# Kernel optimization log

Hardware: AMD Instinct MI355X
Metric: run time of the kernel (lower is better)

## Reference

```python
import jax, jax.numpy as jnp
import numpy as np

B, S, P, V, D = 8, 32, 8, 8000, 128
CONC = 5.0  # concentrator_factor
EPS = 1e-8  # torch cosine_similarity eps


def setup_inputs() -> dict:
    key = jax.random.key(0)
    ks = jax.random.split(key, 8)
    concepts = jax.random.randint(ks[0], (B, S, P), 0, V)
    concepts_length = jax.random.randint(ks[1], (B, S), 0, P + 1)
    seg_len = jax.random.randint(ks[2], (B,), 1, S + 1)
    embed_w = jax.random.normal(ks[3], (V, D), jnp.float32)
    embed_kb_w = jax.random.normal(ks[4], (V, D), jnp.float32)
    edge_matrix = jax.random.uniform(ks[5], (V, V), jnp.float32)
    affectiveness = jax.random.uniform(ks[6], (V,), jnp.float32)
    lam = jnp.full((V,), 0.5, jnp.float32)  # _lambda init to GAW
    return dict(concepts=concepts, concepts_length=concepts_length, seg_len=seg_len,
                embed_w=embed_w, embed_kb_w=embed_kb_w, edge_matrix=edge_matrix,
                affectiveness=affectiveness, lam=lam)


def reference(concepts, concepts_length, seg_len, embed_w, embed_kb_w,
              edge_matrix, affectiveness, lam):
    f32 = embed_w.dtype
    # init_params: normalize edge_matrix rows by their range
    rng = edge_matrix.max(axis=1) - edge_matrix.min(axis=1)  # [V]
    em = edge_matrix / (rng + (rng == 0).astype(f32))[:, None]

    ce = embed_w[concepts]  # [B,S,P,D]
    # ragged mean over P (empty -> zeros, matching empty_tensor)
    pmask = (jnp.arange(P)[None, None, :] < concepts_length[:, :, None]).astype(f32)  # [B,S,P]
    denom = jnp.maximum(concepts_length, 1).astype(f32)[:, :, None]  # [B,S,1]
    mean_j = (ce * pmask[..., None]).sum(axis=2) / denom  # [B,S,D]
    # mean over valid segments j < seg_len
    smask = (jnp.arange(S)[None, :] < seg_len[:, None]).astype(f32)  # [B,S]
    context = (mean_j * smask[..., None]).sum(axis=1) / seg_len.astype(f32)[:, None]  # [B,D]

    # abs cosine similarity vs KB embedding table
    cn = context / jnp.maximum(jnp.linalg.norm(context, axis=1, keepdims=True), EPS)
    kn = embed_kb_w / jnp.maximum(jnp.linalg.norm(embed_kb_w, axis=1, keepdims=True), EPS)
    cos = jnp.abs(cn @ kn.T)  # [B,V]

    eg = em[concepts]  # [B,S,P,V] irregular row gather
    rel = eg * cos[:, None, None, :]
    aff = (eg > 0).astype(f32) * affectiveness
    w = lam * rel + (1.0 - lam) * aff  # [B,S,P,V]
    attn = jax.nn.softmax(w * CONC, axis=3)
    ce2 = attn @ embed_kb_w  # [B,S,P,D]

    # ragged mean over P again, zero out segments j >= seg_len (padded output)
    out = (ce2 * pmask[..., None]).sum(axis=2) / denom  # [B,S,D]
    out = out * smask[..., None]
    return out
```

## Files before the change

kernel.cpp:

```cpp
#include <hip/hip_runtime.h>
#include <cmath>

#define NB 8
#define NS 32
#define NP 8
#define NV 8000
#define ND 128
#define CONC 5.0f
#define EPS 1e-8f

#define TROWS 16
#define USPLIT 25
#define URANGE 320
#define UCHUNK 64
#define NCHUNK (URANGE / UCHUNK)
#define ST 20
#define MAXSLOTS (NB * NS * NP)

#define WS_CNT    0
#define WS_METAO  16
#define WS_SCALE  2064
#define WS_CN     4112
#define WS_COS    5136
#define WS_MEANJ  69136
#define WS_P      101904

__global__ void k_mean(const int* __restrict__ concepts,
                       const int* __restrict__ concepts_length,
                       const float* __restrict__ embed_w,
                       float* __restrict__ mean_j,
                       float* __restrict__ out,
                       int* __restrict__ counter) {
    const int bs = blockIdx.x;
    const int d = threadIdx.x;
    out[bs * ND + d] = 0.0f;
    if (bs == 0 && d == 0) counter[0] = 0;
    const int len = concepts_length[bs];
    float sum = 0.0f;
    for (int p = 0; p < len; ++p) {
        const int c = concepts[bs * NP + p];
        sum += embed_w[(size_t)c * ND + d];
    }
    mean_j[(size_t)bs * ND + d] = sum / (float)(len > 0 ? len : 1);
}

__global__ void k_ctx2(const int* __restrict__ seg_len,
                       const float* __restrict__ mean_j,
                       float* __restrict__ cn) {
    const int b = blockIdx.x;
    const int d = threadIdx.x;
    const int sl = seg_len[b];
    float acc = 0.0f;
    for (int s = 0; s < sl; ++s) acc += mean_j[(size_t)(b * NS + s) * ND + d];
    acc /= (float)sl;
    float ss = acc * acc;
    #pragma unroll
    for (int m = 1; m < 64; m <<= 1) ss += __shfl_xor(ss, m);
    __shared__ float sred[2];
    if ((d & 63) == 0) sred[d >> 6] = ss;
    __syncthreads();
    const float tot = sred[0] + sred[1];
    cn[b * ND + d] = acc / fmaxf(sqrtf(tot), EPS);
}

__global__ __launch_bounds__(256) void k_cos(const float* __restrict__ kb,
                                             const float* __restrict__ cn,
                                             float* __restrict__ cos_bv) {
    __shared__ float s_cn[NB * ND];
    const int t = threadIdx.x;
    for (int i = t; i < NB * ND; i += 256) s_cn[i] = cn[i];
    __syncthreads();

    const int v = blockIdx.x * 8 + (t >> 5);
    const int l = t & 31;
    const float4 kv = *reinterpret_cast<const float4*>(kb + (size_t)v * ND + (l << 2));
    float ss = kv.x * kv.x + kv.y * kv.y + kv.z * kv.z + kv.w * kv.w;
    #pragma unroll
    for (int m = 1; m < 32; m <<= 1) ss += __shfl_xor(ss, m);
    const float inv = 1.0f / fmaxf(sqrtf(ss), EPS);
    #pragma unroll
    for (int b = 0; b < NB; ++b) {
        const float4 cv = *reinterpret_cast<const float4*>(&s_cn[b * ND + (l << 2)]);
        float dot = kv.x * cv.x + kv.y * cv.y + kv.z * cv.z + kv.w * cv.w;
        #pragma unroll
        for (int m = 1; m < 32; m <<= 1) dot += __shfl_xor(dot, m);
        if (l == 0) cos_bv[b * NV + v] = fabsf(dot * inv);
    }
}

__global__ __launch_bounds__(256) void k_A(
        const int* __restrict__ concepts,
        const int* __restrict__ concepts_length,
        const int* __restrict__ seg_len,
        const float* __restrict__ edge,
        const float* __restrict__ aff,
        const float* __restrict__ lam,
        const float* __restrict__ cos_bv,
        int* __restrict__ counter,
        int* __restrict__ meta_out,
        float* __restrict__ f_scale,
        float* __restrict__ pbuf) {
    const int idx = blockIdx.x;
    const int b = idx >> 8;
    const int s = (idx >> 3) & 31;
    const int p = idx & 7;
    if (s >= seg_len[b]) return;
    const int len = concepts_length[b * NS + s];
    if (p >= len) return;
    const int c = concepts[idx];

    const int t = threadIdx.x;
    const float* __restrict__ erow = edge + (size_t)c * NV;
    float4 ev[8];
    float lmax = -INFINITY, lmin = INFINITY;
    #pragma unroll
    for (int k = 0; k < 8; ++k) {
        const int f = t + (k << 8);
        if (f < 2000) {
            const float4 e = *reinterpret_cast<const float4*>(erow + (f << 2));
            ev[k] = e;
            lmax = fmaxf(lmax, fmaxf(fmaxf(e.x, e.y), fmaxf(e.z, e.w)));
            lmin = fminf(lmin, fminf(fminf(e.x, e.y), fminf(e.z, e.w)));
        }
    }
    #pragma unroll
    for (int m = 1; m < 64; m <<= 1) {
        lmax = fmaxf(lmax, __shfl_xor(lmax, m));
        lmin = fminf(lmin, __shfl_xor(lmin, m));
    }
    __shared__ float s_mn[4], s_mx[4], s_sum[4];
    __shared__ int s_slot;
    if (t == 0) s_slot = atomicAdd(counter, 1);
    if ((t & 63) == 0) { s_mn[t >> 6] = lmin; s_mx[t >> 6] = lmax; }
    __syncthreads();
    const float rmin = fminf(fminf(s_mn[0], s_mn[1]), fminf(s_mn[2], s_mn[3]));
    const float rmax = fmaxf(fmaxf(s_mx[0], s_mx[1]), fmaxf(s_mx[2], s_mx[3]));
    const int slot = s_slot;
    const float rng = rmax - rmin;
    const float inv_rng = 1.0f / (rng + (rng == 0.0f ? 1.0f : 0.0f));

    const float* __restrict__ cosb = cos_bv + b * NV;
    float* __restrict__ prow = pbuf + (size_t)slot * NV;
    float lsum = 0.0f;
    #pragma unroll
    for (int k = 0; k < 8; ++k) {
        const int f = t + (k << 8);
        if (f < 2000) {
            const int u = f << 2;
            const float4 l4 = *reinterpret_cast<const float4*>(lam + u);
            const float4 a4 = *reinterpret_cast<const float4*>(aff + u);
            const float4 c4 = *reinterpret_cast<const float4*>(cosb + u);
            float4 e = ev[k];
            e.x *= inv_rng; e.y *= inv_rng; e.z *= inv_rng; e.w *= inv_rng;
            float4 pe;
            pe.x = __expf((l4.x * e.x * c4.x + (1.0f - l4.x) * ((e.x > 0.0f) ? 1.0f : 0.0f) * a4.x) * CONC);
            pe.y = __expf((l4.y * e.y * c4.y + (1.0f - l4.y) * ((e.y > 0.0f) ? 1.0f : 0.0f) * a4.y) * CONC);
            pe.z = __expf((l4.z * e.z * c4.z + (1.0f - l4.z) * ((e.z > 0.0f) ? 1.0f : 0.0f) * a4.z) * CONC);
            pe.w = __expf((l4.w * e.w * c4.w + (1.0f - l4.w) * ((e.w > 0.0f) ? 1.0f : 0.0f) * a4.w) * CONC);
            *reinterpret_cast<float4*>(prow + (f << 2)) = pe;
            lsum += pe.x + pe.y + pe.z + pe.w;
        }
    }
    #pragma unroll
    for (int m = 1; m < 64; m <<= 1) lsum += __shfl_xor(lsum, m);
    if ((t & 63) == 0) s_sum[t >> 6] = lsum;
    __syncthreads();
    if (t == 0) {
        const float total = s_sum[0] + s_sum[1] + s_sum[2] + s_sum[3];
        meta_out[slot] = b * NS + s;
        f_scale[slot] = 1.0f / (total * (float)len);
    }
}

__global__ __launch_bounds__(256) void k_B(
        const float* __restrict__ kb,
        const int* __restrict__ counter,
        const int* __restrict__ meta_out,
        const float* __restrict__ f_scale,
        const float* __restrict__ pbuf,
        float* __restrict__ out) {
    const int count = counter[0];
    const int tile = blockIdx.x;
    if (tile * TROWS >= count) return;

    const int t = threadIdx.x;
    const int ug = t & 7;
    const int l = t >> 3;

    __shared__ int s_o[TROWS];
    __shared__ float s_sc[TROWS];
    __shared__ __align__(16) float s_p[UCHUNK * ST];

    if (t < TROWS) {
        const int slot = tile * TROWS + t;
        s_o[t]  = (slot < count) ? meta_out[slot] : 0;
        s_sc[t] = (slot < count) ? f_scale[slot] : 0.0f;
    }

    const int u0 = blockIdx.y * URANGE;
    const int srow = t >> 4;
    const int sq = t & 15;
    const int prow_ok = (tile * TROWS + srow) < count;
    const float* __restrict__ pr = pbuf + (size_t)(tile * TROWS + srow) * NV;

    float4 acc[TROWS];
    #pragma unroll
    for (int j = 0; j < TROWS; ++j) acc[j] = make_float4(0.f, 0.f, 0.f, 0.f);

    float4 pv = make_float4(0.f, 0.f, 0.f, 0.f);
    if (prow_ok) pv = *reinterpret_cast<const float4*>(pr + u0 + (sq << 2));

    for (int ch = 0; ch < NCHUNK; ++ch) {
        const int uu0 = sq << 2;
        s_p[(uu0 + 0) * ST + srow] = pv.x;
        s_p[(uu0 + 1) * ST + srow] = pv.y;
        s_p[(uu0 + 2) * ST + srow] = pv.z;
        s_p[(uu0 + 3) * ST + srow] = pv.w;
        float4 pnext = make_float4(0.f, 0.f, 0.f, 0.f);
        if (ch + 1 < NCHUNK && prow_ok)
            pnext = *reinterpret_cast<const float4*>(pr + u0 + (ch + 1) * UCHUNK + (sq << 2));
        __syncthreads();

        const int uc = u0 + ch * UCHUNK;
        #pragma unroll
        for (int r = 0; r < 8; ++r) {
            const int uu = ug + (r << 3);
            const float4 kv = *reinterpret_cast<const float4*>(
                kb + (size_t)(uc + uu) * ND + (l << 2));
            const float4 p0 = *reinterpret_cast<const float4*>(&s_p[uu * ST]);
            const float4 p1 = *reinterpret_cast<const float4*>(&s_p[uu * ST + 4]);
            const float4 p2 = *reinterpret_cast<const float4*>(&s_p[uu * ST + 8]);
            const float4 p3 = *reinterpret_cast<const float4*>(&s_p[uu * ST + 12]);
            acc[ 0].x = fmaf(p0.x, kv.x, acc[ 0].x); acc[ 0].y = fmaf(p0.x, kv.y, acc[ 0].y);
            acc[ 0].z = fmaf(p0.x, kv.z, acc[ 0].z); acc[ 0].w = fmaf(p0.x, kv.w, acc[ 0].w);
            acc[ 1].x = fmaf(p0.y, kv.x, acc[ 1].x); acc[ 1].y = fmaf(p0.y, kv.y, acc[ 1].y);
            acc[ 1].z = fmaf(p0.y, kv.z, acc[ 1].z); acc[ 1].w = fmaf(p0.y, kv.w, acc[ 1].w);
            acc[ 2].x = fmaf(p0.z, kv.x, acc[ 2].x); acc[ 2].y = fmaf(p0.z, kv.y, acc[ 2].y);
            acc[ 2].z = fmaf(p0.z, kv.z, acc[ 2].z); acc[ 2].w = fmaf(p0.z, kv.w, acc[ 2].w);
            acc[ 3].x = fmaf(p0.w, kv.x, acc[ 3].x); acc[ 3].y = fmaf(p0.w, kv.y, acc[ 3].y);
            acc[ 3].z = fmaf(p0.w, kv.z, acc[ 3].z); acc[ 3].w = fmaf(p0.w, kv.w, acc[ 3].w);
            acc[ 4].x = fmaf(p1.x, kv.x, acc[ 4].x); acc[ 4].y = fmaf(p1.x, kv.y, acc[ 4].y);
            acc[ 4].z = fmaf(p1.x, kv.z, acc[ 4].z); acc[ 4].w = fmaf(p1.x, kv.w, acc[ 4].w);
            acc[ 5].x = fmaf(p1.y, kv.x, acc[ 5].x); acc[ 5].y = fmaf(p1.y, kv.y, acc[ 5].y);
            acc[ 5].z = fmaf(p1.y, kv.z, acc[ 5].z); acc[ 5].w = fmaf(p1.y, kv.w, acc[ 5].w);
            acc[ 6].x = fmaf(p1.z, kv.x, acc[ 6].x); acc[ 6].y = fmaf(p1.z, kv.y, acc[ 6].y);
            acc[ 6].z = fmaf(p1.z, kv.z, acc[ 6].z); acc[ 6].w = fmaf(p1.z, kv.w, acc[ 6].w);
            acc[ 7].x = fmaf(p1.w, kv.x, acc[ 7].x); acc[ 7].y = fmaf(p1.w, kv.y, acc[ 7].y);
            acc[ 7].z = fmaf(p1.w, kv.z, acc[ 7].z); acc[ 7].w = fmaf(p1.w, kv.w, acc[ 7].w);
            acc[ 8].x = fmaf(p2.x, kv.x, acc[ 8].x); acc[ 8].y = fmaf(p2.x, kv.y, acc[ 8].y);
            acc[ 8].z = fmaf(p2.x, kv.z, acc[ 8].z); acc[ 8].w = fmaf(p2.x, kv.w, acc[ 8].w);
            acc[ 9].x = fmaf(p2.y, kv.x, acc[ 9].x); acc[ 9].y = fmaf(p2.y, kv.y, acc[ 9].y);
            acc[ 9].z = fmaf(p2.y, kv.z, acc[ 9].z); acc[ 9].w = fmaf(p2.y, kv.w, acc[ 9].w);
            acc[10].x = fmaf(p2.z, kv.x, acc[10].x); acc[10].y = fmaf(p2.z, kv.y, acc[10].y);
            acc[10].z = fmaf(p2.z, kv.z, acc[10].z); acc[10].w = fmaf(p2.z, kv.w, acc[10].w);
            acc[11].x = fmaf(p2.w, kv.x, acc[11].x); acc[11].y = fmaf(p2.w, kv.y, acc[11].y);
            acc[11].z = fmaf(p2.w, kv.z, acc[11].z); acc[11].w = fmaf(p2.w, kv.w, acc[11].w);
            acc[12].x = fmaf(p3.x, kv.x, acc[12].x); acc[12].y = fmaf(p3.x, kv.y, acc[12].y);
            acc[12].z = fmaf(p3.x, kv.z, acc[12].z); acc[12].w = fmaf(p3.x, kv.w, acc[12].w);
            acc[13].x = fmaf(p3.y, kv.x, acc[13].x); acc[13].y = fmaf(p3.y, kv.y, acc[13].y);
            acc[13].z = fmaf(p3.y, kv.z, acc[13].z); acc[13].w = fmaf(p3.y, kv.w, acc[13].w);
            acc[14].x = fmaf(p3.z, kv.x, acc[14].x); acc[14].y = fmaf(p3.z, kv.y, acc[14].y);
            acc[14].z = fmaf(p3.z, kv.z, acc[14].z); acc[14].w = fmaf(p3.z, kv.w, acc[14].w);
            acc[15].x = fmaf(p3.w, kv.x, acc[15].x); acc[15].y = fmaf(p3.w, kv.y, acc[15].y);
            acc[15].z = fmaf(p3.w, kv.z, acc[15].z); acc[15].w = fmaf(p3.w, kv.w, acc[15].w);
        }
        __syncthreads();
        pv = pnext;
    }

    float4 r0 = make_float4(0.f, 0.f, 0.f, 0.f);
    float4 r1 = make_float4(0.f, 0.f, 0.f, 0.f);
    #pragma unroll
    for (int j = 0; j < TROWS; ++j) {
        float4 a = acc[j];
        #pragma unroll
        for (int m = 1; m <= 4; m <<= 1) {
            a.x += __shfl_xor(a.x, m);
            a.y += __shfl_xor(a.y, m);
            a.z += __shfl_xor(a.z, m);
            a.w += __shfl_xor(a.w, m);
        }
        if ((j & 7) == ug) { if (j < 8) r0 = a; else r1 = a; }
    }

    const int slot0 = tile * TROWS + ug;
    const int slot1 = slot0 + 8;
    if (slot0 < count) {
        const float sc = s_sc[ug];
        float* o = out + (size_t)s_o[ug] * ND + (l << 2);
        atomicAdd(o + 0, r0.x * sc);
        atomicAdd(o + 1, r0.y * sc);
        atomicAdd(o + 2, r0.z * sc);
        atomicAdd(o + 3, r0.w * sc);
    }
    if (slot1 < count) {
        const float sc = s_sc[ug + 8];
        float* o = out + (size_t)s_o[ug + 8] * ND + (l << 2);
        atomicAdd(o + 0, r1.x * sc);
        atomicAdd(o + 1, r1.y * sc);
        atomicAdd(o + 2, r1.z * sc);
        atomicAdd(o + 3, r1.w * sc);
    }
}

extern "C" void kernel_launch(void* const* d_in, const int* in_sizes, int n_in,
                              void* d_out, int out_size, void* d_ws, size_t ws_size,
                              hipStream_t stream) {
    const int*   concepts        = (const int*)d_in[0];
    const int*   concepts_length = (const int*)d_in[1];
    const int*   seg_len         = (const int*)d_in[2];
    const float* embed_w         = (const float*)d_in[3];
    const float* embed_kb_w      = (const float*)d_in[4];
    const float* edge_matrix     = (const float*)d_in[5];
    const float* affectiveness   = (const float*)d_in[6];
    const float* lam             = (const float*)d_in[7];
    float* out = (float*)d_out;

    float* wsf = (float*)d_ws;
    int*   wsi = (int*)d_ws;
    int*   counter  = wsi + WS_CNT;
    int*   meta_out = wsi + WS_METAO;
    float* f_scale  = wsf + WS_SCALE;
    float* cn       = wsf + WS_CN;
    float* cos_bv   = wsf + WS_COS;
    float* mean_j   = wsf + WS_MEANJ;
    float* pbuf     = wsf + WS_P;

    k_mean<<<NB * NS, ND, 0, stream>>>(concepts, concepts_length, embed_w,
                                       mean_j, out, counter);
    k_ctx2<<<NB, ND, 0, stream>>>(seg_len, mean_j, cn);
    k_cos<<<NV / 8, 256, 0, stream>>>(embed_kb_w, cn, cos_bv);
    k_A<<<MAXSLOTS, 256, 0, stream>>>(concepts, concepts_length, seg_len,
                                      edge_matrix, affectiveness, lam, cos_bv,
                                      counter, meta_out, f_scale, pbuf);
    dim3 gB(MAXSLOTS / TROWS, USPLIT, 1);
    k_B<<<gB, 256, 0, stream>>>(embed_kb_w, counter, meta_out, f_scale, pbuf, out);
}
```

Measured before the change: 437.0 us.

## Pre-reduce softmax rows over P before the KB matmul, drop atomic slot compaction

Uses linearity to scale and sum each segment's softmax numerator rows over P while staging them into shared memory. The matmul against the KB table then runs with 8 segment rows per tile instead of 16 concept rows. It also drops the atomic slot counter and compacted metadata and indexes pbuf directly by (b,s,p), skipping tiles whose segments are past seg_len. This cuts matmul FLOPs and output atomics, at the cost of more scattered pbuf loads per thread and lost compaction when many slots are empty.

Result: faster. 367.8 us (-15.8%).

```diff
diff --git a/kernel.cpp b/kernel.cpp
--- a/kernel.cpp
+++ b/kernel.cpp
@@ -9,32 +9,29 @@
 #define CONC 5.0f
 #define EPS 1e-8f
 
-#define TROWS 16
+#define NBS (NB * NS)
+#define TROWS 8
 #define USPLIT 25
 #define URANGE 320
 #define UCHUNK 64
 #define NCHUNK (URANGE / UCHUNK)
-#define ST 20
-#define MAXSLOTS (NB * NS * NP)
-
-#define WS_CNT    0
-#define WS_METAO  16
-#define WS_SCALE  2064
-#define WS_CN     4112
-#define WS_COS    5136
-#define WS_MEANJ  69136
-#define WS_P      101904
+#define ST 12
+#define MAXIDX (NB * NS * NP)
+
+#define WS_SCALE  0
+#define WS_CN     2048
+#define WS_COS    3072
+#define WS_MEANJ  67072
+#define WS_P      99840
 
 __global__ void k_mean(const int* __restrict__ concepts,
                        const int* __restrict__ concepts_length,
                        const float* __restrict__ embed_w,
                        float* __restrict__ mean_j,
-                       float* __restrict__ out,
-                       int* __restrict__ counter) {
+                       float* __restrict__ out) {
     const int bs = blockIdx.x;
     const int d = threadIdx.x;
     out[bs * ND + d] = 0.0f;
-    if (bs == 0 && d == 0) counter[0] = 0;
     const int len = concepts_length[bs];
     float sum = 0.0f;
     for (int p = 0; p < len; ++p) {
@@ -96,8 +93,6 @@
         const float* __restrict__ aff,
         const float* __restrict__ lam,
         const float* __restrict__ cos_bv,
-        int* __restrict__ counter,
-        int* __restrict__ meta_out,
         float* __restrict__ f_scale,
         float* __restrict__ pbuf) {
     const int idx = blockIdx.x;
@@ -129,18 +124,15 @@
         lmin = fminf(lmin, __shfl_xor(lmin, m));
     }
     __shared__ float s_mn[4], s_mx[4], s_sum[4];
-    __shared__ int s_slot;
-    if (t == 0) s_slot = atomicAdd(counter, 1);
     if ((t & 63) == 0) { s_mn[t >> 6] = lmin; s_mx[t >> 6] = lmax; }
     __syncthreads();
     const float rmin = fminf(fminf(s_mn[0], s_mn[1]), fminf(s_mn[2], s_mn[3]));
     const float rmax = fmaxf(fmaxf(s_mx[0], s_mx[1]), fmaxf(s_mx[2], s_mx[3]));
-    const int slot = s_slot;
     const float rng = rmax - rmin;
     const float inv_rng = 1.0f / (rng + (rng == 0.0f ? 1.0f : 0.0f));
 
     const float* __restrict__ cosb = cos_bv + b * NV;
-    float* __restrict__ prow = pbuf + (size_t)slot * NV;
+    float* __restrict__ prow = pbuf + (size_t)idx * NV;
     float lsum = 0.0f;
     #pragma unroll
     for (int k = 0; k < 8; ++k) {
@@ -167,58 +159,78 @@
     __syncthreads();
     if (t == 0) {
         const float total = s_sum[0] + s_sum[1] + s_sum[2] + s_sum[3];
-        meta_out[slot] = b * NS + s;
-        f_scale[slot] = 1.0f / (total * (float)len);
+        f_scale[idx] = 1.0f / (total * (float)len);
     }
 }
 
 __global__ __launch_bounds__(256) void k_B(
         const float* __restrict__ kb,
-        const int* __restrict__ counter,
-        const int* __restrict__ meta_out,
+        const int* __restrict__ seg_len,
+        const int* __restrict__ concepts_length,
         const float* __restrict__ f_scale,
         const float* __restrict__ pbuf,
         float* __restrict__ out) {
-    const int count = counter[0];
     const int tile = blockIdx.x;
-    if (tile * TROWS >= count) return;
+    const int bs0 = tile * TROWS;
+    if ((bs0 & 31) >= seg_len[bs0 >> 5]) return;
 
     const int t = threadIdx.x;
     const int ug = t & 7;
     const int l = t >> 3;
 
-    __shared__ int s_o[TROWS];
-    __shared__ float s_sc[TROWS];
+    __shared__ int   s_ln[TROWS];
+    __shared__ float s_sc[TROWS * NP];
     __shared__ __align__(16) float s_p[UCHUNK * ST];
 
     if (t < TROWS) {
-        const int slot = tile * TROWS + t;
-        s_o[t]  = (slot < count) ? meta_out[slot] : 0;
-        s_sc[t] = (slot < count) ? f_scale[slot] : 0.0f;
-    }
-
+        const int bs = bs0 + t;
+        s_ln[t] = ((bs & 31) < seg_len[bs >> 5]) ? concepts_length[bs] : 0;
+    }
+    if (t < TROWS * NP) {
+        const int bs = bs0 + (t >> 3);
+        const int p = t & 7;
+        const bool valid = ((bs & 31) < seg_len[bs >> 5]) && (p < concepts_length[bs]);
+        s_sc[t] = valid ? f_scale[bs * NP + p] : 0.0f;
+    }
+    __syncthreads();
+
+    const int srow = t >> 5;
+    const int sq = t & 31;
+    const int lenr = s_ln[srow];
+    float scr[NP];
+    #pragma unroll
+    for (int p = 0; p < NP; ++p) scr[p] = s_sc[srow * NP + p];
+    const float* __restrict__ pr = pbuf + (size_t)(bs0 + srow) * NP * NV + (sq << 1);
     const int u0 = blockIdx.y * URANGE;
-    const int srow = t >> 4;
-    const int sq = t & 15;
-    const int prow_ok = (tile * TROWS + srow) < count;
-    const float* __restrict__ pr = pbuf + (size_t)(tile * TROWS + srow) * NV;
 
     float4 acc[TROWS];
     #pragma unroll
     for (int j = 0; j < TROWS; ++j) acc[j] = make_float4(0.f, 0.f, 0.f, 0.f);
 
-    float4 pv = make_float4(0.f, 0.f, 0.f, 0.f);
-    if (prow_ok) pv = *reinterpret_cast<const float4*>(pr + u0 + (sq << 2));
+    float2 pv = make_float2(0.f, 0.f);
+    #pragma unroll
+    for (int p = 0; p < NP; ++p)
+        if (p < lenr) {
+            const float2 v = *reinterpret_cast<const float2*>(pr + (size_t)p * NV + u0);
+            pv.x = fmaf(scr[p], v.x, pv.x);
+            pv.y = fmaf(scr[p], v.y, pv.y);
+        }
 
     for (int ch = 0; ch < NCHUNK; ++ch) {
-        const int uu0 = sq << 2;
+        const int uu0 = sq << 1;
         s_p[(uu0 + 0) * ST + srow] = pv.x;
         s_p[(uu0 + 1) * ST + srow] = pv.y;
-        s_p[(uu0 + 2) * ST + srow] = pv.z;
-        s_p[(uu0 + 3) * ST + srow] = pv.w;
-        float4 pnext = make_float4(0.f, 0.f, 0.f, 0.f);
-        if (ch + 1 < NCHUNK && prow_ok)
-            pnext = *reinterpret_cast<const float4*>(pr + u0 + (ch + 1) * UCHUNK + (sq << 2));
+        float2 pn = make_float2(0.f, 0.f);
+        if (ch + 1 < NCHUNK) {
+            const int off = u0 + (ch + 1) * UCHUNK;
+            #pragma unroll
+            for (int p = 0; p < NP; ++p)
+                if (p < lenr) {
+                    const float2 v = *reinterpret_cast<const float2*>(pr + (size_t)p * NV + off);
+                    pn.x = fmaf(scr[p], v.x, pn.x);
+                    pn.y = fmaf(scr[p], v.y, pn.y);
+                }
+        }
         __syncthreads();
 
         const int uc = u0 + ch * UCHUNK;
@@ -229,47 +241,28 @@
                 kb + (size_t)(uc + uu) * ND + (l << 2));
             const float4 p0 = *reinterpret_cast<const float4*>(&s_p[uu * ST]);
             const float4 p1 = *reinterpret_cast<const float4*>(&s_p[uu * ST + 4]);
-            const float4 p2 = *reinterpret_cast<const float4*>(&s_p[uu * ST + 8]);
-            const float4 p3 = *reinterpret_cast<const float4*>(&s_p[uu * ST + 12]);
-            acc[ 0].x = fmaf(p0.x, kv.x, acc[ 0].x); acc[ 0].y = fmaf(p0.x, kv.y, acc[ 0].y);
-            acc[ 0].z = fmaf(p0.x, kv.z, acc[ 0].z); acc[ 0].w = fmaf(p0.x, kv.w, acc[ 0].w);
-            acc[ 1].x = fmaf(p0.y, kv.x, acc[ 1].x); acc[ 1].y = fmaf(p0.y, kv.y, acc[ 1].y);
-            acc[ 1].z = fmaf(p0.y, kv.z, acc[ 1].z); acc[ 1].w = fmaf(p0.y, kv.w, acc[ 1].w);
-            acc[ 2].x = fmaf(p0.z, kv.x, acc[ 2].x); acc[ 2].y = fmaf(p0.z, kv.y, acc[ 2].y);
-            acc[ 2].z = fmaf(p0.z, kv.z, acc[ 2].z); acc[ 2].w = fmaf(p0.z, kv.w, acc[ 2].w);
-            acc[ 3].x = fmaf(p0.w, kv.x, acc[ 3].x); acc[ 3].y = fmaf(p0.w, kv.y, acc[ 3].y);
-            acc[ 3].z = fmaf(p0.w, kv.z, acc[ 3].z); acc[ 3].w = fmaf(p0.w, kv.w, acc[ 3].w);
-            acc[ 4].x = fmaf(p1.x, kv.x, acc[ 4].x); acc[ 4].y = fmaf(p1.x, kv.y, acc[ 4].y);
-            acc[ 4].z = fmaf(p1.x, kv.z, acc[ 4].z); acc[ 4].w = fmaf(p1.x, kv.w, acc[ 4].w);
-            acc[ 5].x = fmaf(p1.y, kv.x, acc[ 5].x); acc[ 5].y = fmaf(p1.y, kv.y, acc[ 5].y);
-            acc[ 5].z = fmaf(p1.y, kv.z, acc[ 5].z); acc[ 5].w = fmaf(p1.y, kv.w, acc[ 5].w);
-            acc[ 6].x = fmaf(p1.z, kv.x, acc[ 6].x); acc[ 6].y = fmaf(p1.z, kv.y, acc[ 6].y);
-            acc[ 6].z = fmaf(p1.z, kv.z, acc[ 6].z); acc[ 6].w = fmaf(p1.z, kv.w, acc[ 6].w);
-            acc[ 7].x = fmaf(p1.w, kv.x, acc[ 7].x); acc[ 7].y = fmaf(p1.w, kv.y, acc[ 7].y);
-            acc[ 7].z = fmaf(p1.w, kv.z, acc[ 7].z); acc[ 7].w = fmaf(p1.w, kv.w, acc[ 7].w);
-            acc[ 8].x = fmaf(p2.x, kv.x, acc[ 8].x); acc[ 8].y = fmaf(p2.x, kv.y, acc[ 8].y);
-            acc[ 8].z = fmaf(p2.x, kv.z, acc[ 8].z); acc[ 8].w = fmaf(p2.x, kv.w, acc[ 8].w);
-            acc[ 9].x = fmaf(p2.y, kv.x, acc[ 9].x); acc[ 9].y = fmaf(p2.y, kv.y, acc[ 9].y);
-            acc[ 9].z = fmaf(p2.y, kv.z, acc[ 9].z); acc[ 9].w = fmaf(p2.y, kv.w, acc[ 9].w);
-            acc[10].x = fmaf(p2.z, kv.x, acc[10].x); acc[10].y = fmaf(p2.z, kv.y, acc[10].y);
-            acc[10].z = fmaf(p2.z, kv.z, acc[10].z); acc[10].w = fmaf(p2.z, kv.w, acc[10].w);
-            acc[11].x = fmaf(p2.w, kv.x, acc[11].x); acc[11].y = fmaf(p2.w, kv.y, acc[11].y);
-            acc[11].z = fmaf(p2.w, kv.z, acc[11].z); acc[11].w = fmaf(p2.w, kv.w, acc[11].w);
-            acc[12].x = fmaf(p3.x, kv.x, acc[12].x); acc[12].y = fmaf(p3.x, kv.y, acc[12].y);
-            acc[12].z = fmaf(p3.x, kv.z, acc[12].z); acc[12].w = fmaf(p3.x, kv.w, acc[12].w);
-            acc[13].x = fmaf(p3.y, kv.x, acc[13].x); acc[13].y = fmaf(p3.y, kv.y, acc[13].y);
-            acc[13].z = fmaf(p3.y, kv.z, acc[13].z); acc[13].w = fmaf(p3.y, kv.w, acc[13].w);
-            acc[14].x = fmaf(p3.z, kv.x, acc[14].x); acc[14].y = fmaf(p3.z, kv.y, acc[14].y);
-            acc[14].z = fmaf(p3.z, kv.z, acc[14].z); acc[14].w = fmaf(p3.z, kv.w, acc[14].w);
-            acc[15].x = fmaf(p3.w, kv.x, acc[15].x); acc[15].y = fmaf(p3.w, kv.y, acc[15].y);
-            acc[15].z = fmaf(p3.w, kv.z, acc[15].z); acc[15].w = fmaf(p3.w, kv.w, acc[15].w);
+            acc[0].x = fmaf(p0.x, kv.x, acc[0].x); acc[0].y = fmaf(p0.x, kv.y, acc[0].y);
+            acc[0].z = fmaf(p0.x, kv.z, acc[0].z); acc[0].w = fmaf(p0.x, kv.w, acc[0].w);
+            acc[1].x = fmaf(p0.y, kv.x, acc[1].x); acc[1].y = fmaf(p0.y, kv.y, acc[1].y);
+            acc[1].z = fmaf(p0.y, kv.z, acc[1].z); acc[1].w = fmaf(p0.y, kv.w, acc[1].w);
+            acc[2].x = fmaf(p0.z, kv.x, acc[2].x); acc[2].y = fmaf(p0.z, kv.y, acc[2].y);
+            acc[2].z = fmaf(p0.z, kv.z, acc[2].z); acc[2].w = fmaf(p0.z, kv.w, acc[2].w);
+            acc[3].x = fmaf(p0.w, kv.x, acc[3].x); acc[3].y = fmaf(p0.w, kv.y, acc[3].y);
+            acc[3].z = fmaf(p0.w, kv.z, acc[3].z); acc[3].w = fmaf(p0.w, kv.w, acc[3].w);
+            acc[4].x = fmaf(p1.x, kv.x, acc[4].x); acc[4].y = fmaf(p1.x, kv.y, acc[4].y);
+            acc[4].z = fmaf(p1.x, kv.z, acc[4].z); acc[4].w = fmaf(p1.x, kv.w, acc[4].w);
+            acc[5].x = fmaf(p1.y, kv.x, acc[5].x); acc[5].y = fmaf(p1.y, kv.y, acc[5].y);
+            acc[5].z = fmaf(p1.y, kv.z, acc[5].z); acc[5].w = fmaf(p1.y, kv.w, acc[5].w);
+            acc[6].x = fmaf(p1.z, kv.x, acc[6].x); acc[6].y = fmaf(p1.z, kv.y, acc[6].y);
+            acc[6].z = fmaf(p1.z, kv.z, acc[6].z); acc[6].w = fmaf(p1.z, kv.w, acc[6].w);
+            acc[7].x = fmaf(p1.w, kv.x, acc[7].x); acc[7].y = fmaf(p1.w, kv.y, acc[7].y);
+            acc[7].z = fmaf(p1.w, kv.z, acc[7].z); acc[7].w = fmaf(p1.w, kv.w, acc[7].w);
         }
         __syncthreads();
-        pv = pnext;
+        pv = pn;
     }
 
     float4 r0 = make_float4(0.f, 0.f, 0.f, 0.f);
-    float4 r1 = make_float4(0.f, 0.f, 0.f, 0.f);
     #pragma unroll
     for (int j = 0; j < TROWS; ++j) {
         float4 a = acc[j];
@@ -280,26 +273,15 @@
             a.z += __shfl_xor(a.z, m);
             a.w += __shfl_xor(a.w, m);
         }
-        if ((j & 7) == ug) { if (j < 8) r0 = a; else r1 = a; }
-    }
-
-    const int slot0 = tile * TROWS + ug;
-    const int slot1 = slot0 + 8;
-    if (slot0 < count) {
-        const float sc = s_sc[ug];
-        float* o = out + (size_t)s_o[ug] * ND + (l << 2);
-        atomicAdd(o + 0, r0.x * sc);
-        atomicAdd(o + 1, r0.y * sc);
-        atomicAdd(o + 2, r0.z * sc);
-        atomicAdd(o + 3, r0.w * sc);
-    }
-    if (slot1 < count) {
-        const float sc = s_sc[ug + 8];
-        float* o = out + (size_t)s_o[ug + 8] * ND + (l << 2);
-        atomicAdd(o + 0, r1.x * sc);
-        atomicAdd(o + 1, r1.y * sc);
-        atomicAdd(o + 2, r1.z * sc);
-        atomicAdd(o + 3, r1.w * sc);
+        if (j == ug) r0 = a;
+    }
+
+    if (s_ln[ug] != 0) {
+        float* o = out + (size_t)(bs0 + ug) * ND + (l << 2);
+        atomicAdd(o + 0, r0.x);
+        atomicAdd(o + 1, r0.y);
+        atomicAdd(o + 2, r0.z);
+        atomicAdd(o + 3, r0.w);
     }
 }
 
@@ -317,9 +299,6 @@
     float* out = (float*)d_out;
 
     float* wsf = (float*)d_ws;
-    int*   wsi = (int*)d_ws;
-    int*   counter  = wsi + WS_CNT;
-    int*   meta_out = wsi + WS_METAO;
     float* f_scale  = wsf + WS_SCALE;
     float* cn       = wsf + WS_CN;
     float* cos_bv   = wsf + WS_COS;
@@ -327,12 +306,13 @@
     float* pbuf     = wsf + WS_P;
 
     k_mean<<<NB * NS, ND, 0, stream>>>(concepts, concepts_length, embed_w,
-                                       mean_j, out, counter);
+                                       mean_j, out);
     k_ctx2<<<NB, ND, 0, stream>>>(seg_len, mean_j, cn);
     k_cos<<<NV / 8, 256, 0, stream>>>(embed_kb_w, cn, cos_bv);
-    k_A<<<MAXSLOTS, 256, 0, stream>>>(concepts, concepts_length, seg_len,
-                                      edge_matrix, affectiveness, lam, cos_bv,
-                                      counter, meta_out, f_scale, pbuf);
-    dim3 gB(MAXSLOTS / TROWS, USPLIT, 1);
-    k_B<<<gB, 256, 0, stream>>>(embed_kb_w, counter, meta_out, f_scale, pbuf, out);
-}
+    k_A<<<MAXIDX, 256, 0, stream>>>(concepts, concepts_length, seg_len,
+                                    edge_matrix, affectiveness, lam, cos_bv,
+                                    f_scale, pbuf);
+    dim3 gB(NBS / TROWS, USPLIT, 1);
+    k_B<<<gB, 256, 0, stream>>>(embed_kb_w, seg_len, concepts_length,
+                                f_scale, pbuf, out);
+}
```
